# Kernel tuning notes

Hardware: AMD Instinct MI355X
Metric: run time of the kernel (lower is better)

## Reference

```python
import jax, jax.numpy as jnp
import numpy as np

N, E, G = 8192, 65536, 16          # nodes, edges, graphs
EMBED, HID, L = 512, 1024, 3       # embed_dim, hidden_dim, hidden_layers
NG, RBF_R = 50, 12.0               # num_gaussians, rbf_radius
AVG_LEN = 60.0
IN_DIM = 3 * EMBED


def _mlp_params(key, in_dim, hid, out_dim, n_layers):
    ks = jax.random.split(key, 6)
    s_in = 1.0 / np.sqrt(in_dim)
    s_h = 1.0 / np.sqrt(hid)
    return dict(
        in_w=jax.random.normal(ks[0], (in_dim, hid), jnp.float32) * s_in,
        in_b=jnp.zeros((hid,), jnp.float32),
        hid_w=jax.random.normal(ks[1], (n_layers, hid, hid), jnp.float32) * s_h,
        hid_b=jnp.zeros((n_layers, hid), jnp.float32),
        out_w=jax.random.normal(ks[2], (hid, out_dim), jnp.float32) * s_h,
        out_b=jnp.zeros((out_dim,), jnp.float32),
    )


def setup_inputs() -> dict:
    key = jax.random.key(0)
    k = jax.random.split(key, 8)
    x = jax.random.normal(k[0], (N, EMBED), jnp.float32)
    edge_index = jax.random.randint(k[1], (2, E), 0, N, dtype=jnp.int32)
    batch = jnp.sort(jax.random.randint(k[2], (N,), 0, G, dtype=jnp.int32))
    dist = jax.random.uniform(k[3], (E,), jnp.float32) * RBF_R
    v = jax.random.normal(k[4], (E, 3), jnp.float32)
    vec_hat = v / jnp.linalg.norm(v, axis=-1, keepdims=True)
    rbf_w = jax.random.normal(k[5], (NG, EMBED), jnp.float32) * (1.0 / np.sqrt(NG))
    rbf_b = jnp.zeros((EMBED,), jnp.float32)
    e = _mlp_params(k[6], IN_DIM, HID, 1, L)
    f = _mlp_params(k[7], IN_DIM, HID, 1, L)
    return dict(
        x=x, edge_index=edge_index, batch=batch, dist=dist, vec_hat=vec_hat,
        rbf_w=rbf_w, rbf_b=rbf_b,
        e_in_w=e['in_w'], e_in_b=e['in_b'], e_hid_w=e['hid_w'], e_hid_b=e['hid_b'], e_out_w=e['out_w'], e_out_b=e['out_b'],
        f_in_w=f['in_w'], f_in_b=f['in_b'], f_hid_w=f['hid_w'], f_hid_b=f['hid_b'], f_out_w=f['out_w'], f_out_b=f['out_b'],
    )


def _res_mlp(h_in, in_w, in_b, hid_w, hid_b, out_w, out_b):
    h = jax.nn.silu(h_in @ in_w + in_b)           # [E, HID]
    for i in range(L):                             # residual hidden blocks
        h = h + jax.nn.silu(h @ hid_w[i] + hid_b[i])
    return h @ out_w + out_b                       # [E, 1]


def _rbf(dist, rbf_w, rbf_b):
    offsets = jnp.linspace(0.0, RBF_R, NG)
    coeff = -0.5 / (offsets[1] - offsets[0]) ** 2
    g = jnp.exp(coeff * (dist[:, None] - offsets) ** 2)  # [E, NG]
    return g @ rbf_w + rbf_b                              # [E, EMBED]


def reference(x, edge_index, batch, dist, vec_hat,
              rbf_w, rbf_b,
              e_in_w, e_in_b, e_hid_w, e_hid_b, e_out_w, e_out_b,
              f_in_w, f_in_b, f_hid_w, f_hid_b, f_out_w, f_out_b):
    src, dst = edge_index[0], edge_index[1]
    rbf = _rbf(dist, rbf_w, rbf_b)                                 # [E, EMBED]
    inputs = jnp.concatenate([x[src], x[dst], rbf], axis=-1)       # [E, 3*EMBED]
    energy_pairs = _res_mlp(inputs, e_in_w, e_in_b, e_hid_w, e_hid_b, e_out_w, e_out_b)  # [E,1]
    force_pairs = _res_mlp(inputs, f_in_w, f_in_b, f_hid_w, f_hid_b, f_out_w, f_out_b) * vec_hat  # [E,3]
    energy = jax.ops.segment_sum(energy_pairs, batch[src], num_segments=G) / (AVG_LEN ** 2)  # [G,1]
    forces = jax.ops.segment_sum(force_pairs, src, num_segments=N) / AVG_LEN                 # [N,3]
    return energy, forces
```

## Files before the change

### kernel.cpp

```cpp
#include <hip/hip_runtime.h>
#include <math.h>

#define NUM_E 65536
#define NUM_N 8192
#define NUM_G 16
#define RBFR 12.0f

typedef unsigned short u16;
typedef _Float16 f16x8 __attribute__((ext_vector_type(8)));
typedef _Float16 f16x4 __attribute__((ext_vector_type(4)));
typedef float f32x4 __attribute__((ext_vector_type(4)));

#define TILE_F16 8192
#define L1SZ   1114112
#define HSZ    1048576
#define MSTRIDE 4259840

#define FU1  139264
#define FUHL 131072
#define FUPM (FU1 + 3 * FUHL)

#define GLD16(gp, lp) __builtin_amdgcn_global_load_lds( \
    (const __attribute__((address_space(1))) void*)(gp), \
    (__attribute__((address_space(3))) void*)(lp), 16, 0, 0)

#define VMW12() asm volatile("s_waitcnt vmcnt(12)" ::: "memory")
#define VMW10() asm volatile("s_waitcnt vmcnt(10)" ::: "memory")
#define VMW8()  asm volatile("s_waitcnt vmcnt(8)" ::: "memory")
#define VMW0()  asm volatile("s_waitcnt vmcnt(0)" ::: "memory")
#define BARX()  __builtin_amdgcn_s_barrier()

__global__ void wrbf_kernel(const float* __restrict__ rbf_w, const float* __restrict__ rbf_b,
                            const float* __restrict__ e_in_w, const float* __restrict__ e_in_b,
                            const float* __restrict__ f_in_w, const float* __restrict__ f_in_b,
                            float* __restrict__ wrbf_e, float* __restrict__ b1_e,
                            float* __restrict__ wrbf_f, float* __restrict__ b1_f) {
  int blk = blockIdx.x;
  int mlp = blk / 204;
  int rr = blk % 204;
  int row = rr >> 2;
  int ns = rr & 3;
  const float* in_w = mlp ? f_in_w : e_in_w;
  const float* in_b = mlp ? f_in_b : e_in_b;
  float* wrbf = mlp ? wrbf_f : wrbf_e;
  float* b1   = mlp ? b1_f : b1_e;
  __shared__ float vec[512];
  __shared__ float4 red[256];
  int tid = threadIdx.x;
  vec[tid]       = (row < 50) ? rbf_w[row * 512 + tid]       : rbf_b[tid];
  vec[tid + 256] = (row < 50) ? rbf_w[row * 512 + tid + 256] : rbf_b[tid + 256];
  __syncthreads();
  int q = tid >> 6, l = tid & 63;
  int n0 = ns * 256 + l * 4;
  float a0 = 0.f, a1 = 0.f, a2 = 0.f, a3 = 0.f;
  for (int c = q * 128; c < q * 128 + 128; ++c) {
    float4 wv = *(const float4*)&in_w[(size_t)(1024 + c) * 1024 + n0];
    float gv = vec[c];
    a0 += gv * wv.x; a1 += gv * wv.y; a2 += gv * wv.z; a3 += gv * wv.w;
  }
  red[tid] = float4{a0, a1, a2, a3};
  __syncthreads();
  if (q == 0) {
    float4 s0 = red[l], s1 = red[l + 64], s2 = red[l + 128], s3 = red[l + 192];
    float4 o = {s0.x + s1.x + s2.x + s3.x, s0.y + s1.y + s2.y + s3.y,
                s0.z + s1.z + s2.z + s3.z, s0.w + s1.w + s2.w + s3.w};
    if (row < 50) {
      *(float4*)&wrbf[row * 1024 + n0] = o;
    } else {
      o.x += in_b[n0]; o.y += in_b[n0 + 1]; o.z += in_b[n0 + 2]; o.w += in_b[n0 + 3];
      *(float4*)&b1[n0] = o;
    }
  }
}

__global__ void xh_kernel(const float* __restrict__ x, u16* __restrict__ xh) {
  int i = blockIdx.x * 256 + threadIdx.x;
  float4 v = ((const float4*)x)[i];
  f16x4 h = {(_Float16)v.x, (_Float16)v.y, (_Float16)v.z, (_Float16)v.w};
  *(f16x4*)(xh + (size_t)i * 4) = h;
}

__global__ void grbf_kernel(const float* __restrict__ dist, u16* __restrict__ grbf) {
  int u = blockIdx.x * 256 + threadIdx.x;
  int e = u >> 3, q = u & 7;
  const float delta = RBFR / 49.f;
  const float coeff = -0.5f / (delta * delta);
  float d = dist[e];
  f16x8 h;
#pragma unroll
  for (int j = 0; j < 8; ++j) {
    int gi = q * 8 + j;
    float dd = d - (float)gi * delta;
    float gg = (gi < 50) ? __expf(coeff * dd * dd) : 0.f;
    h[j] = (_Float16)gg;
  }
  *(f16x8*)(grbf + (size_t)u * 8) = h;
}

__global__ void pack_gemm(const float* __restrict__ e_in_w, const float* __restrict__ e_hid_w,
                          const float* __restrict__ f_in_w, const float* __restrict__ f_hid_w,
                          const float* __restrict__ wrbf_e, const float* __restrict__ wrbf_f,
                          u16* __restrict__ wp) {
  int u = blockIdx.x * 256 + threadIdx.x;
  if (u >= 2 * (MSTRIDE / 8)) return;
  int mlpi = (u >= MSTRIDE / 8) ? 1 : 0;
  int v = u - mlpi * (MSTRIDE / 8);
  const float* in_w  = mlpi ? f_in_w : e_in_w;
  const float* hid_w = mlpi ? f_hid_w : e_hid_w;
  const float* wrbf  = mlpi ? wrbf_f : wrbf_e;
  int t = v >> 10;
  int unit = v & 1023;
  int n_loc = unit >> 3;
  int sp = unit & 7;
  int ks = sp ^ (n_loc & 7);
  f16x8 vals;
  if (t < 136) {
    int grp = t / 17;
    int kt = t % 17;
    int bnp = grp >> 1, nhp = grp & 1;
    int n = bnp * 256 + ((n_loc >> 5) << 6) + nhp * 32 + (n_loc & 31);
    int k0 = kt * 64 + ks * 8;
#pragma unroll
    for (int j = 0; j < 8; ++j) {
      int k = k0 + j;
      float f = (k < 1024) ? in_w[(size_t)k * 1024 + n]
              : ((k < 1074) ? wrbf[(k - 1024) * 1024 + n] : 0.f);
      vals[j] = (_Float16)f;
    }
  } else {
    int th = t - 136;
    int lay = th >> 7;
    int t2 = th & 127;
    int bnp = t2 >> 5;
    int nhp = (t2 >> 4) & 1;
    int kt = t2 & 15;
    int n = bnp * 256 + ((n_loc >> 5) << 6) + nhp * 32 + (n_loc & 31);
    int k0 = kt * 64 + ks * 8;
#pragma unroll
    for (int j = 0; j < 8; ++j)
      vals[j] = (_Float16)hid_w[(size_t)((lay << 10) + k0 + j) * 1024 + n];
  }
  *(f16x8*)(wp + (size_t)mlpi * MSTRIDE + (size_t)t * TILE_F16 + unit * 8) = vals;
}


#define STA(b, ah, kt) do { \
  _Pragma("unroll") for (int _j = 0; _j < 2; ++_j) { \
    int _ck = wv * 2 + _j; \
    int _loc = _ck * 8 + (lane >> 3); \
    int _row = ((_loc >> 6) << 7) + (ah) * 64 + (_loc & 63); \
    int _sw = ((lane & 7) ^ (_loc & 7)) << 3; \
    const u16* _gp; \
    if (MODE == 1) { \
      if ((kt) < 16) { \
        int _nd = ((kt) < 8) ? s_src[_row] : s_dst[_row]; \
        _gp = hin + ((size_t)_nd * 512 + ((kt) & 7) * 64 + _sw); \
      } else { \
        _gp = grbf + ((size_t)(eg0 + _row) * 64 + _sw); \
      } \
    } else { \
      _gp = hin + ((size_t)(rowb + _row) * 1024 + (kt) * 64 + _sw); \
    } \
    GLD16(_gp, (char*)&sm[b][ah][0] + _ck * 1024); \
  } \
} while (0)

#define STB(b, bh, kt) do { \
  const u16* _wt = wl + ((size_t)((bn * 2 + (bh)) * NKT + (kt))) * TILE_F16; \
  _Pragma("unroll") for (int _j = 0; _j < 2; ++_j) { \
    int _ck = wv * 2 + _j; \
    GLD16(_wt + _ck * 512 + lane * 8, (char*)&sm[b][2 + (bh)][0] + _ck * 1024); \
  } \
} while (0)

#define RDA(b, mh) do { \
  _Pragma("unroll") for (int _ks = 0; _ks < 2; ++_ks) { \
    int _kk = _ks * 4 + (lane >> 4); \
    _Pragma("unroll") for (int _m = 0; _m < 4; ++_m) { \
      int _r = wm * 64 + _m * 16 + (lane & 15); \
      af[_m][_ks] = *(const f16x8*)&sm[b][mh][_r * 64 + ((_kk ^ (_r & 7)) << 3)]; \
    } \
  } \
} while (0)

#define RDB(b, nh) do { \
  _Pragma("unroll") for (int _ks = 0; _ks < 2; ++_ks) { \
    int _kk = _ks * 4 + (lane >> 4); \
    _Pragma("unroll") for (int _n = 0; _n < 2; ++_n) { \
      int _c = wn * 32 + _n * 16 + (lane & 15); \
      bf[nh][_n][_ks] = *(const f16x8*)&sm[b][2 + (nh)][_c * 64 + ((_kk ^ (_c & 7)) << 3)]; \
    } \
  } \
} while (0)

#define PHM(mh, nh) do { \
  __builtin_amdgcn_s_setprio(1); \
  _Pragma("unroll") for (int _ks = 0; _ks < 2; ++_ks) \
    _Pragma("unroll") for (int _m = 0; _m < 4; ++_m) \
      _Pragma("unroll") for (int _n = 0; _n < 2; ++_n) \
        acc[(mh) * 4 + _m][(nh) * 2 + _n] = __builtin_amdgcn_mfma_f32_16x16x32_f16( \
            bf[nh][_n][_ks], af[_m][_ks], acc[(mh) * 4 + _m][(nh) * 2 + _n], 0, 0, 0); \
  __builtin_amdgcn_s_setprio(0); \
} while (0)

template<int NKT, int MODE>
__global__ __launch_bounds__(512, 2) void gemm8k(
    const u16* __restrict__ hinE, const u16* __restrict__ hinF,
    const u16* __restrict__ grbf, const int* __restrict__ eidx,
    const int* __restrict__ batch, const float* __restrict__ vhat,
    const u16* __restrict__ wp, size_t woff,
    const float* __restrict__ biasE, const float* __restrict__ biasF,
    u16* __restrict__ houtE, u16* __restrict__ houtF,
    const float* __restrict__ owE, const float* __restrict__ owF,
    const float* __restrict__ obE, const float* __restrict__ obF,
    float* __restrict__ out, int mstart) {
  __shared__ __align__(16) u16 sm[2][4][8192];
  __shared__ int s_src[256];
  __shared__ int s_dst[256];
  __shared__ float sred[256];
  __shared__ float sbins[16];
  const int tid = threadIdx.x;
  const int lane = tid & 63;
  const int wv = tid >> 6;
  const int wm = wv >> 2, wn = wv & 3;

  int mlp, mt, bn;
  if (MODE == 1) {
    int g = (blockIdx.x & 7) * (gridDim.x >> 3) + (blockIdx.x >> 3);
    mt = g >> 3;
    int bnq = g & 7;
    mlp = bnq >> 2;
    bn = bnq & 3;
  } else {
    mlp = blockIdx.x & 1;
    int b2 = blockIdx.x >> 1;
    int g = (b2 & 7) * ((gridDim.x >> 1) >> 3) + (b2 >> 3);
    mt = g >> 2;
    bn = g & 3;
  }
  const u16* hin = (MODE == 1) ? hinE : (mlp ? hinF : hinE);
  const u16* wl = wp + (size_t)mlp * MSTRIDE + woff;
  const float* bias = mlp ? biasF : biasE;
  u16* hout = mlp ? houtF : houtE;
  const int rowb = mt * 256;
  const int n0 = bn * 256;
  const int eg0 = mstart + rowb;

  if (MODE == 1) {
    if (tid < 256) s_src[tid] = eidx[eg0 + tid];
    else s_dst[tid - 256] = eidx[NUM_E + eg0 + tid - 256];
    __syncthreads();
  }

  f32x4 acc[8][4];
#pragma unroll
  for (int m = 0; m < 8; ++m)
#pragma unroll
    for (int n = 0; n < 4; ++n)
#pragma unroll
      for (int i = 0; i < 4; ++i) acc[m][n][i] = 0.f;

  f16x8 af[4][2], bf[2][2][2];

  STA(0, 0, 0); STB(0, 0, 0); STB(0, 1, 0); STA(0, 1, 0);

  for (int t = 0; t < NKT - 1; ++t) {
    const int b = t & 1, nb = b ^ 1;
    STA(nb, 0, t + 1); STB(nb, 0, t + 1); STB(nb, 1, t + 1); STA(nb, 1, t + 1);
    VMW12(); BARX();
    RDA(b, 0); RDB(b, 0);
    PHM(0, 0); BARX();
    VMW10(); BARX();
    RDB(b, 1);
    PHM(0, 1); BARX();
    VMW8(); BARX();
    RDA(b, 1);
    PHM(1, 0); BARX();
    PHM(1, 1); BARX();
  }
  {
    const int tb = (NKT - 1) & 1;
    VMW0(); BARX();
    RDA(tb, 0); RDB(tb, 0); PHM(0, 0);
    RDB(tb, 1); PHM(0, 1);
    RDA(tb, 1); PHM(1, 0); PHM(1, 1);
  }

  if (MODE != 2) {
#pragma unroll
    for (int mi = 0; mi < 8; ++mi) {
#pragma unroll
      for (int ni = 0; ni < 4; ++ni) {
        int grow = rowb + wm * 128 + mi * 16 + (lane & 15);
        int gn = n0 + wn * 64 + ni * 16 + ((lane >> 4) << 2);
        float4 bi = *(const float4*)&bias[gn];
        f16x4 o;
        if (MODE == 1) {
#pragma unroll
          for (int i = 0; i < 4; ++i) {
            float pre = acc[mi][ni][i] + ((const float*)&bi)[i];
            o[i] = (_Float16)(pre / (1.f + __expf(-pre)));
          }
        } else {
          f16x4 hp = *(const f16x4*)&hin[(size_t)grow * 1024 + gn];
#pragma unroll
          for (int i = 0; i < 4; ++i) {
            float pre = acc[mi][ni][i] + ((const float*)&bi)[i];
            o[i] = (_Float16)(pre / (1.f + __expf(-pre)) + (float)hp[i]);
          }
        }
        *(f16x4*)&hout[(size_t)grow * 1024 + gn] = o;
      }
    }
  } else {
    if (tid < 256) sred[tid] = 0.f;
    if (tid < 16) sbins[tid] = 0.f;
    __syncthreads();
    const float* ow = mlp ? owF : owE;
    float p[8];
#pragma unroll
    for (int mi = 0; mi < 8; ++mi) p[mi] = 0.f;
#pragma unroll
    for (int mi = 0; mi < 8; ++mi) {
#pragma unroll
      for (int ni = 0; ni < 4; ++ni) {
        int grow = rowb + wm * 128 + mi * 16 + (lane & 15);
        int gn = n0 + wn * 64 + ni * 16 + ((lane >> 4) << 2);
        float4 bi = *(const float4*)&bias[gn];
        float4 wv4 = *(const float4*)&ow[gn];
        f16x4 hp = *(const f16x4*)&hin[(size_t)grow * 1024 + gn];
#pragma unroll
        for (int i = 0; i < 4; ++i) {
          float pre = acc[mi][ni][i] + ((const float*)&bi)[i];
          float val = pre / (1.f + __expf(-pre)) + (float)hp[i];
          p[mi] += val * ((const float*)&wv4)[i];
        }
      }
    }
#pragma unroll
    for (int mi = 0; mi < 8; ++mi) {
      p[mi] += __shfl_down(p[mi], 32, 64);
      p[mi] += __shfl_down(p[mi], 16, 64);
    }
    if ((lane >> 4) == 0) {
#pragma unroll
      for (int mi = 0; mi < 8; ++mi)
        atomicAdd(&sred[wm * 128 + mi * 16 + (lane & 15)], p[mi]);
    }
    __syncthreads();
    if (tid < 256) {
      float s = sred[tid];
      int eg = eg0 + tid;
      int si = eidx[eg];
      if (mlp == 0) {
        float pv = s + ((bn == 0) ? obE[0] : 0.f);
        atomicAdd(&sbins[batch[si]], pv);
      } else {
        float pv = (s + ((bn == 0) ? obF[0] : 0.f)) * (1.f / 60.f);
        atomicAdd(&out[16 + si * 3 + 0], pv * vhat[(size_t)eg * 3 + 0]);
        atomicAdd(&out[16 + si * 3 + 1], pv * vhat[(size_t)eg * 3 + 1]);
        atomicAdd(&out[16 + si * 3 + 2], pv * vhat[(size_t)eg * 3 + 2]);
      }
    }
    __syncthreads();
    if (mlp == 0 && tid < 16) atomicAdd(&out[tid], sbins[tid] * (1.f / 3600.f));
  }
}

#define FSWZ(row, col) ((((row) * 1088) + (col)) ^ (((row) & 7) << 3))

__global__ void packF_kernel(const float* __restrict__ e_in_w, const float* __restrict__ e_hid_w,
                             const float* __restrict__ f_in_w, const float* __restrict__ f_hid_w,
                             const float* __restrict__ wrbf_e, const float* __restrict__ wrbf_f,
                             u16* __restrict__ wp) {
  int u = blockIdx.x * 256 + threadIdx.x;
  if (u >= 2 * FUPM) return;
  int m = (u >= FUPM) ? 1 : 0;
  int v = u - m * FUPM;
  const float* in_w  = m ? f_in_w : e_in_w;
  const float* hid_w = m ? f_hid_w : e_hid_w;
  const float* wrbf  = m ? wrbf_f : wrbf_e;
  int l = v & 63;
  int kb = (l >> 4) << 3;
  f16x8 vals;
  if (v < FU1) {
    int kt = v >> 12;
    int ntg = (v >> 6) & 63;
    int n = ntg * 16 + (l & 15);
    int k0 = kt * 32 + kb;
#pragma unroll
    for (int jj = 0; jj < 8; ++jj) {
      int k = k0 + jj;
      float f = (k < 1024) ? in_w[(size_t)k * 1024 + n]
              : ((k < 1074) ? wrbf[(k - 1024) * 1024 + n] : 0.f);
      vals[jj] = (_Float16)f;
    }
  } else {
    int vh = v - FU1;
    int lay = vh >> 17;
    int kt = (vh >> 12) & 31;
    int ntg = (vh >> 6) & 63;
    int n = ntg * 16 + (l & 15);
    int k0 = kt * 32 + kb;
#pragma unroll
    for (int jj = 0; jj < 8; ++jj)
      vals[jj] = (_Float16)hid_w[(size_t)((lay << 10) + k0 + jj) * 1024 + n];
  }
  *(f16x8*)(wp + (size_t)u * 8) = vals;
}

#define F_LOADB(buf, kt) do { \
  const u16* _wr = wl + ((size_t)((kt) * 64 + wave * 8) * 64 + lane) * 8; \
  _Pragma("unroll") \
  for (int _nt = 0; _nt < 8; ++_nt) buf[_nt] = *(const f16x8*)(_wr + (size_t)_nt * 512); \
} while (0)
#define F_LOADA(buf, kt) do { \
  const int _kb = (kt) * 32 + ((lane >> 4) << 3); \
  _Pragma("unroll") \
  for (int _r = 0; _r < 4; ++_r) buf[_r] = *(const f16x8*)&Alds[FSWZ(_r * 16 + (lane & 15), _kb)]; \
} while (0)
#define F_MFMAS(abuf, bbuf) do { \
  _Pragma("unroll") \
  for (int _nt = 0; _nt < 8; ++_nt) \
    _Pragma("unroll") \
    for (int _r = 0; _r < 4; ++_r) \
      acc[_r][_nt] = __builtin_amdgcn_mfma_f32_16x16x32_f16(abuf[_r], bbuf[_nt], acc[_r][_nt], 0, 0, 0); \
} while (0)

__global__ __launch_bounds__(512, 2) void fusedF_kernel(
    const float* __restrict__ x, const int* __restrict__ eidx,
    const int* __restrict__ batch, const float* __restrict__ dist,
    const float* __restrict__ vhat,
    const u16* __restrict__ wp,
    const float* __restrict__ b1_e, const float* __restrict__ b1_f,
    const float* __restrict__ e_hid_b, const float* __restrict__ f_hid_b,
    const float* __restrict__ e_out_w, const float* __restrict__ e_out_b,
    const float* __restrict__ f_out_w, const float* __restrict__ f_out_b,
    float* __restrict__ out) {
  __shared__ __align__(16) u16 Alds[64 * 1088];
  __shared__ float sow[1024];
  __shared__ float sbins[16];
  __shared__ int s_src[64];
  __shared__ int s_dst[64];
  __shared__ float s_dist[64];
  const int tid = threadIdx.x;
  const int lane = tid & 63;
  const int wave = tid >> 6;
  const int e0 = blockIdx.x * 64;
  if (tid < 16) sbins[tid] = 0.f;
  if (tid < 64) s_src[tid] = eidx[e0 + tid];
  if (tid >= 64 && tid < 128) s_dst[tid - 64] = eidx[NUM_E + e0 + tid - 64];
  if (tid >= 128 && tid < 192) s_dist[tid - 128] = dist[e0 + tid - 128];
  __syncthreads();
  const float delta = RBFR / 49.f;
  const float coeff = -0.5f / (delta * delta);
  for (int mlp = 0; mlp < 2; ++mlp) {
    for (int i = tid; i < 16384; i += 512) {
      int e = i >> 8;
      int part = (i >> 7) & 1;
      int q = i & 127;
      int nrow = part ? s_dst[e] : s_src[e];
      float4 v = ((const float4*)x)[(size_t)nrow * 128 + q];
      int col = part * 512 + q * 4;
      f16x4 hv = {(_Float16)v.x, (_Float16)v.y, (_Float16)v.z, (_Float16)v.w};
      *(f16x4*)&Alds[FSWZ(e, col)] = hv;
    }
    for (int i = tid; i < 4096; i += 512) {
      int e = i >> 6;
      int gi = i & 63;
      float d = s_dist[e] - (float)gi * delta;
      float g2 = (gi < 50) ? __expf(coeff * d * d) : 0.f;
      _Float16 hg = (_Float16)g2;
      Alds[FSWZ(e, 1024 + gi)] = __builtin_bit_cast(u16, hg);
    }
    __syncthreads();
    const u16* wp1 = wp + (size_t)mlp * FUPM * 8;
    const u16* wph = wp1 + (size_t)FU1 * 8;
    const float* b1 = mlp ? b1_f : b1_e;
    const float* hb = mlp ? f_hid_b : e_hid_b;
    for (int layer = 0; layer < 4; ++layer) {
      const int nkt = (layer == 0) ? 34 : 32;
      const u16* wl = (layer == 0) ? wp1 : (wph + (size_t)(layer - 1) * FUHL * 8);
      const float* bias = (layer == 0) ? b1 : (hb + (layer - 1) * 1024);
      f32x4 acc[4][8];
#pragma unroll
      for (int r = 0; r < 4; ++r)
#pragma unroll
        for (int nt = 0; nt < 8; ++nt)
#pragma unroll
          for (int i = 0; i < 4; ++i) acc[r][nt][i] = 0.f;
      f16x8 a0[4], a1[4], b0[8], b1r[8];
      F_LOADA(a0, 0); F_LOADB(b0, 0);
      F_LOADA(a1, 1); F_LOADB(b1r, 1);
      for (int kt = 0; kt < nkt; kt += 2) {
        F_MFMAS(a0, b0);
        if (kt + 2 < nkt) { F_LOADA(a0, kt + 2); F_LOADB(b0, kt + 2); }
        F_MFMAS(a1, b1r);
        if (kt + 3 < nkt) { F_LOADA(a1, kt + 3); F_LOADB(b1r, kt + 3); }
      }
      __syncthreads();
      float bia[8];
#pragma unroll
      for (int nt = 0; nt < 8; ++nt) bia[nt] = bias[wave * 128 + nt * 16 + (lane & 15)];
#pragma unroll
      for (int r = 0; r < 4; ++r) {
#pragma unroll
        for (int nt = 0; nt < 8; ++nt) {
#pragma unroll
          for (int i = 0; i < 4; ++i) {
            int row = r * 16 + ((lane >> 4) << 2) + i;
            int col = wave * 128 + nt * 16 + (lane & 15);
            float pre = acc[r][nt][i] + bia[nt];
            float val = pre / (1.f + __expf(-pre));
            int idx = FSWZ(row, col);
            if (layer > 0) {
              _Float16 oldh = __builtin_bit_cast(_Float16, Alds[idx]);
              val += (float)oldh;
            }
            _Float16 nh = (_Float16)val;
            Alds[idx] = __builtin_bit_cast(u16, nh);
          }
        }
      }
      __syncthreads();
    }
    const float* ow = mlp ? f_out_w : e_out_w;
    for (int i = tid; i < 1024; i += 512) sow[i] = ow[i];
    __syncthreads();
    {
      int e = tid >> 3;
      int part = tid & 7;
      float s = 0.f;
#pragma unroll
      for (int cc = 0; cc < 16; ++cc) {
        int col = part * 128 + cc * 8;
        f16x8 hv = *(const f16x8*)&Alds[FSWZ(e, col)];
#pragma unroll
        for (int q = 0; q < 8; ++q) s += (float)hv[q] * sow[col + q];
      }
      s += __shfl_down(s, 4, 8);
      s += __shfl_down(s, 2, 8);
      s += __shfl_down(s, 1, 8);
      if (part == 0) {
        if (mlp == 0) {
          float pp = s + e_out_b[0];
          int gg = batch[s_src[e]];
          atomicAdd(&sbins[gg], pp);
        } else {
          float pp = (s + f_out_b[0]) * (1.f / 60.f);
          int si = s_src[e];
          atomicAdd(&out[16 + si * 3 + 0], pp * vhat[(size_t)(e0 + e) * 3 + 0]);
          atomicAdd(&out[16 + si * 3 + 1], pp * vhat[(size_t)(e0 + e) * 3 + 1]);
          atomicAdd(&out[16 + si * 3 + 2], pp * vhat[(size_t)(e0 + e) * 3 + 2]);
        }
      }
    }
    __syncthreads();
  }
  if (tid < 16) atomicAdd(&out[tid], sbins[tid] * (1.f / 3600.f));
}

extern "C" void kernel_launch(void* const* d_in, const int* in_sizes, int n_in,
                              void* d_out, int out_size, void* d_ws, size_t ws_size,
                              hipStream_t stream) {
  (void)in_sizes; (void)n_in;
  const float* x      = (const float*)d_in[0];
  const int*   eidx   = (const int*)d_in[1];
  const int*   batch  = (const int*)d_in[2];
  const float* dist   = (const float*)d_in[3];
  const float* vhat   = (const float*)d_in[4];
  const float* rbf_w  = (const float*)d_in[5];
  const float* rbf_b  = (const float*)d_in[6];
  const float* e_in_w = (const float*)d_in[7];
  const float* e_in_b = (const float*)d_in[8];
  const float* e_hid_w = (const float*)d_in[9];
  const float* e_hid_b = (const float*)d_in[10];
  const float* e_out_w = (const float*)d_in[11];
  const float* e_out_b = (const float*)d_in[12];
  const float* f_in_w = (const float*)d_in[13];
  const float* f_in_b = (const float*)d_in[14];
  const float* f_hid_w = (const float*)d_in[15];
  const float* f_hid_b = (const float*)d_in[16];
  const float* f_out_w = (const float*)d_in[17];
  const float* f_out_b = (const float*)d_in[18];

  const size_t WP_BYTES = 17039360;
  u16* wp       = (u16*)d_ws;
  float* wrbf_e = (float*)((char*)d_ws + WP_BYTES);
  float* wrbf_f = wrbf_e + 50 * 1024;
  float* b1_e   = wrbf_f + 50 * 1024;
  float* b1_f   = b1_e + 1024;
  const size_t BASE = WP_BYTES + 409600 + 8192;
  u16* xh   = (u16*)((char*)d_ws + BASE);
  u16* grbf = (u16*)((char*)d_ws + BASE + 8388608);
  const size_t FIXED = BASE + 16777216;

  int nch = 0;
  for (int c = 1; c <= 8; c <<= 1) {
    size_t need = FIXED + 4 * (size_t)(NUM_E / c) * 1024 * sizeof(u16);
    if (need <= ws_size) { nch = c; break; }
  }

  hipMemsetAsync(d_out, 0, (size_t)out_size * sizeof(float), stream);
  wrbf_kernel<<<408, 256, 0, stream>>>(rbf_w, rbf_b, e_in_w, e_in_b, f_in_w, f_in_b,
                                       wrbf_e, b1_e, wrbf_f, b1_f);

  if (nch == 0) {
    packF_kernel<<<(2 * FUPM + 255) / 256, 256, 0, stream>>>(
        e_in_w, e_hid_w, f_in_w, f_hid_w, wrbf_e, wrbf_f, wp);
    fusedF_kernel<<<NUM_E / 64, 512, 0, stream>>>(x, eidx, batch, dist, vhat, wp,
                                                  b1_e, b1_f, e_hid_b, f_hid_b,
                                                  e_out_w, e_out_b, f_out_w, f_out_b,
                                                  (float*)d_out);
    return;
  }

  pack_gemm<<<(2 * (MSTRIDE / 8) + 255) / 256, 256, 0, stream>>>(
      e_in_w, e_hid_w, f_in_w, f_hid_w, wrbf_e, wrbf_f, wp);
  xh_kernel<<<(NUM_N * 512 / 4) / 256, 256, 0, stream>>>(x, xh);
  grbf_kernel<<<(NUM_E * 8) / 256, 256, 0, stream>>>(dist, grbf);

  const int Mchunk = NUM_E / nch;
  u16* hE0 = (u16*)((char*)d_ws + FIXED);
  u16* hE1 = hE0 + (size_t)Mchunk * 1024;
  u16* hF0 = hE1 + (size_t)Mchunk * 1024;
  u16* hF1 = hF0 + (size_t)Mchunk * 1024;
  float* out = (float*)d_out;

  for (int c = 0; c < nch; ++c) {
    int mstart = c * Mchunk;
    int grid = Mchunk / 32;
    gemm8k<17, 1><<<grid, 512, 0, stream>>>(
        xh, xh, grbf, eidx, batch, vhat, wp, 0,
        b1_e, b1_f, hE0, hF0, e_out_w, f_out_w, e_out_b, f_out_b, out, mstart);
    gemm8k<16, 0><<<grid, 512, 0, stream>>>(
        hE0, hF0, grbf, eidx, batch, vhat, wp, L1SZ,
        e_hid_b, f_hid_b, hE1, hF1, e_out_w, f_out_w, e_out_b, f_out_b, out, mstart);
    gemm8k<16, 0><<<grid, 512, 0, stream>>>(
        hE1, hF1, grbf, eidx, batch, vhat, wp, L1SZ + HSZ,
        e_hid_b + 1024, f_hid_b + 1024, hE0, hF0, e_out_w, f_out_w, e_out_b, f_out_b, out, mstart);
    gemm8k<16, 2><<<grid, 512, 0, stream>>>(
        hE0, hF0, grbf, eidx, batch, vhat, wp, L1SZ + 2 * HSZ,
        e_hid_b + 2048, f_hid_b + 2048, hE1, hF1, e_out_w, f_out_w, e_out_b, f_out_b, out, mstart);
  }
}
```

Measured before the change: 1.555 ms.

## Interleave GEMM tile prefetch with MFMA phases and stage weight packing through LDS

```diff
diff --git a/kernel.cpp b/kernel.cpp
--- a/kernel.cpp
+++ b/kernel.cpp
@@ -24,9 +24,7 @@
     (const __attribute__((address_space(1))) void*)(gp), \
     (__attribute__((address_space(3))) void*)(lp), 16, 0, 0)
 
-#define VMW12() asm volatile("s_waitcnt vmcnt(12)" ::: "memory")
-#define VMW10() asm volatile("s_waitcnt vmcnt(10)" ::: "memory")
-#define VMW8()  asm volatile("s_waitcnt vmcnt(8)" ::: "memory")
+#define VMW4()  asm volatile("s_waitcnt vmcnt(4)" ::: "memory")
 #define VMW0()  asm volatile("s_waitcnt vmcnt(0)" ::: "memory")
 #define BARX()  __builtin_amdgcn_s_barrier()
 
@@ -101,46 +99,56 @@
                           const float* __restrict__ f_in_w, const float* __restrict__ f_hid_w,
                           const float* __restrict__ wrbf_e, const float* __restrict__ wrbf_f,
                           u16* __restrict__ wp) {
-  int u = blockIdx.x * 256 + threadIdx.x;
-  if (u >= 2 * (MSTRIDE / 8)) return;
-  int mlpi = (u >= MSTRIDE / 8) ? 1 : 0;
-  int v = u - mlpi * (MSTRIDE / 8);
+  __shared__ __align__(16) u16 tile[TILE_F16];
+  int bid = blockIdx.x;
+  int mlpi = (bid >= 520) ? 1 : 0;
+  int t = bid - mlpi * 520;
   const float* in_w  = mlpi ? f_in_w : e_in_w;
   const float* hid_w = mlpi ? f_hid_w : e_hid_w;
   const float* wrbf  = mlpi ? wrbf_f : wrbf_e;
-  int t = v >> 10;
-  int unit = v & 1023;
-  int n_loc = unit >> 3;
-  int sp = unit & 7;
-  int ks = sp ^ (n_loc & 7);
-  f16x8 vals;
+  int tid = threadIdx.x;
+  int kq = tid >> 7;
+  int nl = tid & 127;
+  int n, k0, lay = 0, is_l1;
   if (t < 136) {
     int grp = t / 17;
     int kt = t % 17;
     int bnp = grp >> 1, nhp = grp & 1;
-    int n = bnp * 256 + ((n_loc >> 5) << 6) + nhp * 32 + (n_loc & 31);
-    int k0 = kt * 64 + ks * 8;
-#pragma unroll
-    for (int j = 0; j < 8; ++j) {
-      int k = k0 + j;
-      float f = (k < 1024) ? in_w[(size_t)k * 1024 + n]
-              : ((k < 1074) ? wrbf[(k - 1024) * 1024 + n] : 0.f);
-      vals[j] = (_Float16)f;
-    }
+    n = bnp * 256 + ((nl >> 5) << 6) + nhp * 32 + (nl & 31);
+    k0 = kt * 64;
+    is_l1 = 1;
   } else {
     int th = t - 136;
-    int lay = th >> 7;
+    lay = th >> 7;
     int t2 = th & 127;
-    int bnp = t2 >> 5;
-    int nhp = (t2 >> 4) & 1;
+    int bnp = t2 >> 5, nhp = (t2 >> 4) & 1;
     int kt = t2 & 15;
-    int n = bnp * 256 + ((n_loc >> 5) << 6) + nhp * 32 + (n_loc & 31);
-    int k0 = kt * 64 + ks * 8;
-#pragma unroll
-    for (int j = 0; j < 8; ++j)
-      vals[j] = (_Float16)hid_w[(size_t)((lay << 10) + k0 + j) * 1024 + n];
-  }
-  *(f16x8*)(wp + (size_t)mlpi * MSTRIDE + (size_t)t * TILE_F16 + unit * 8) = vals;
+    n = bnp * 256 + ((nl >> 5) << 6) + nhp * 32 + (nl & 31);
+    k0 = kt * 64;
+    is_l1 = 0;
+  }
+#pragma unroll 8
+  for (int j = 0; j < 32; ++j) {
+    int kk = j * 2 + kq;
+    int k = k0 + kk;
+    float f;
+    if (is_l1) {
+      f = (k < 1024) ? in_w[(size_t)k * 1024 + n]
+        : ((k < 1074) ? wrbf[(k - 1024) * 1024 + n] : 0.f);
+    } else {
+      f = hid_w[(size_t)((lay << 10) + k) * 1024 + n];
+    }
+    int pos = nl * 64 + ((((kk >> 3) ^ (nl & 7)) << 3) | (kk & 7));
+    _Float16 hf = (_Float16)f;
+    tile[pos] = __builtin_bit_cast(u16, hf);
+  }
+  __syncthreads();
+  u16* dst = wp + (size_t)mlpi * MSTRIDE + (size_t)t * TILE_F16;
+#pragma unroll
+  for (int i = 0; i < 4; ++i) {
+    int off = (i * 256 + tid) * 8;
+    *(f16x8*)(dst + off) = *(const f16x8*)(tile + off);
+  }
 }
 
 
@@ -263,20 +271,25 @@
   f16x8 af[4][2], bf[2][2][2];
 
   STA(0, 0, 0); STB(0, 0, 0); STB(0, 1, 0); STA(0, 1, 0);
+  VMW4(); BARX();
 
   for (int t = 0; t < NKT - 1; ++t) {
     const int b = t & 1, nb = b ^ 1;
-    STA(nb, 0, t + 1); STB(nb, 0, t + 1); STB(nb, 1, t + 1); STA(nb, 1, t + 1);
-    VMW12(); BARX();
+    STA(nb, 0, t + 1);
     RDA(b, 0); RDB(b, 0);
-    PHM(0, 0); BARX();
-    VMW10(); BARX();
+    VMW4(); BARX();
+    PHM(0, 0);
+    STB(nb, 0, t + 1);
     RDB(b, 1);
-    PHM(0, 1); BARX();
-    VMW8(); BARX();
+    VMW4(); BARX();
+    PHM(0, 1);
+    STB(nb, 1, t + 1);
     RDA(b, 1);
-    PHM(1, 0); BARX();
-    PHM(1, 1); BARX();
+    VMW4(); BARX();
+    PHM(1, 0);
+    STA(nb, 1, t + 1);
+    VMW4(); BARX();
+    PHM(1, 1);
   }
   {
     const int tb = (NKT - 1) & 1;
@@ -615,7 +628,7 @@
     return;
   }
 
-  pack_gemm<<<(2 * (MSTRIDE / 8) + 255) / 256, 256, 0, stream>>>(
+  pack_gemm<<<1040, 256, 0, stream>>>(
       e_in_w, e_hid_w, f_in_w, f_hid_w, wrbf_e, wrbf_f, wp);
   xh_kernel<<<(NUM_N * 512 / 4) / 256, 256, 0, stream>>>(x, xh);
   grbf_kernel<<<(NUM_E * 8) / 256, 256, 0, stream>>>(dist, grbf);
```

Result: no change. 1.532 ms (-1.5%).
